# Performance work log

Hardware: AMD Instinct MI355X
Metric: run time of the kernel (lower is better)

Reference implementation:

```python
import jax, jax.numpy as jnp
import numpy as np

B, D, H, C = 8192, 384, 256, 6
K_MIN, K_MAX = 4, 16
LN_EPS = 1e-5


def setup_inputs() -> dict:
    key = jax.random.key(0)
    ks = jax.random.split(key, 6)
    s = lambda k, shape: (jax.random.normal(k, shape, jnp.float32) * 0.05)
    return {
        "x": jax.random.normal(ks[0], (B, D), jnp.float32),
        "W_proj": s(ks[1], (D, H)), "b_proj": jnp.zeros((H,), jnp.float32),
        "W_tau": s(ks[2], (D, 1)), "b_tau": jnp.zeros((1,), jnp.float32),
        "W_res": s(ks[3], (H, H)), "b_res": jnp.zeros((H,), jnp.float32),
        "ln_g": jnp.ones((H,), jnp.float32), "ln_b": jnp.zeros((H,), jnp.float32),
        "W_fc": s(ks[4], (H, C)), "b_fc": jnp.zeros((C,), jnp.float32),
    }


def reference(x, W_proj, b_proj, W_tau, b_tau, W_res, b_res, ln_g, ln_b, W_fc, b_fc):
    # adaptive k per sample (torch path casts to int -> non-differentiable)
    tau = jax.nn.sigmoid(x @ W_tau + b_tau)[:, 0]                      # [B]
    k = jax.lax.stop_gradient(
        jnp.clip(jnp.round(K_MAX - (K_MAX - K_MIN) * tau), 1, K_MAX)
    ).astype(jnp.int32)                                                # [B]

    # pairwise squared distances (same nearest-neighbor ordering as cdist)
    sq = jnp.sum(x * x, axis=-1)                                       # [B]
    d2 = sq[:, None] + sq[None, :] - 2.0 * (x @ x.T)                   # [B,B]
    _, idx = jax.lax.top_k(-jax.lax.stop_gradient(d2), K_MAX)          # [B,K_MAX] nearest (incl. self)

    h = jax.nn.relu(x @ W_proj + b_proj)                               # [B,H]

    # ragged top-k mean via fixed K_MAX gather + position mask
    gathered = h[idx]                                                  # [B,K_MAX,H]
    mask = (jnp.arange(K_MAX)[None, :] < k[:, None]).astype(h.dtype)   # [B,K_MAX]
    agg = jnp.einsum('bkh,bk->bh', gathered, mask) / k[:, None].astype(h.dtype)

    r = jax.nn.relu(agg @ W_res + b_res)                               # [B,H]
    z = h + r
    mu = jnp.mean(z, axis=-1, keepdims=True)
    var = jnp.var(z, axis=-1, keepdims=True)
    zn = (z - mu) / jnp.sqrt(var + LN_EPS)
    return (zn * ln_g + ln_b) @ W_fc + b_fc                            # [B,C]
```

## Files before the change

kernel.cpp:

```cpp
#include <hip/hip_runtime.h>
#include <hip/hip_fp16.h>
#include <math.h>

#define NROWS 8192
#define DDIM 384
#define HDIM 256
#define CDIM 6
#define LN_EPS 1e-5f
#define DSTR 138

typedef short bf16x8 __attribute__((ext_vector_type(8)));
typedef float f32x4 __attribute__((ext_vector_type(4)));
typedef unsigned short u16x8 __attribute__((ext_vector_type(8)));
typedef unsigned short u16x4 __attribute__((ext_vector_type(4)));
typedef unsigned short u16x2 __attribute__((ext_vector_type(2)));

__device__ __forceinline__ bool dj_better(float d1, int j1, float d2, int j2) {
    return (d1 < d2) || (d1 == d2 && j1 < j2);
}

__device__ __forceinline__ unsigned int umin_(unsigned int a, unsigned int b) { return a < b ? a : b; }
__device__ __forceinline__ unsigned int umax_(unsigned int a, unsigned int b) { return a > b ? a : b; }

__device__ __forceinline__ unsigned short map16f(float v) {
    union { _Float16 f; unsigned short u; } c;
    c.f = (_Float16)v;
    unsigned short b = c.u;
    return (unsigned short)(b ^ (unsigned short)((((short)b) >> 15) | 0x8000));
}

__device__ __forceinline__ float unmap16(unsigned int m16b) {
    unsigned short fb = (m16b & 0x8000u) ? (unsigned short)(m16b ^ 0x8000u)
                                         : (unsigned short)(~m16b);
    union { unsigned short u; _Float16 f; } cv; cv.u = fb;
    return (float)cv.f;
}

__device__ __forceinline__ unsigned short rne_bf16(float v) {
    unsigned int u = __float_as_uint(v);
    u += 0x7fffu + ((u >> 16) & 1u);
    return (unsigned short)(u >> 16);
}

__device__ __forceinline__ void ins8(
    unsigned int& s0, unsigned int& s1, unsigned int& s2, unsigned int& s3,
    unsigned int& s4, unsigned int& s5, unsigned int& s6, unsigned int& s7,
    unsigned int& m, unsigned int key)
{
    if (key < m) {
        s0 = (s0 == m) ? key : s0;
        s1 = (s1 == m) ? key : s1;
        s2 = (s2 == m) ? key : s2;
        s3 = (s3 == m) ? key : s3;
        s4 = (s4 == m) ? key : s4;
        s5 = (s5 == m) ? key : s5;
        s6 = (s6 == m) ? key : s6;
        s7 = (s7 == m) ? key : s7;
        m = umax_(umax_(umax_(s0, s1), umax_(s2, s3)),
                  umax_(umax_(s4, s5), umax_(s6, s7)));
    }
}

__device__ __forceinline__ unsigned int max8_(
    unsigned int s0, unsigned int s1, unsigned int s2, unsigned int s3,
    unsigned int s4, unsigned int s5, unsigned int s6, unsigned int s7)
{
    return umax_(umax_(umax_(s0, s1), umax_(s2, s3)),
                 umax_(umax_(s4, s5), umax_(s6, s7)));
}

__global__ void __launch_bounds__(256) prep_kernel(
    const float* __restrict__ x, const float* __restrict__ W_tau,
    const float* __restrict__ b_tau, unsigned short* __restrict__ xb,
    float* __restrict__ sq, int* __restrict__ kk,
    const float* __restrict__ Wp, unsigned short* __restrict__ wpT,
    const float* __restrict__ Wr, unsigned short* __restrict__ wrT)
{
    int tid = threadIdx.x;
    if (blockIdx.x < NROWS / 4) {
        int wave = tid >> 6, lane = tid & 63;
        int row = blockIdx.x * 4 + wave;
        const float* xr = x + (size_t)row * DDIM;
        unsigned short* xbr = xb + (size_t)row * DDIM;
        float s = 0.f, tp = 0.f;
        #pragma unroll
        for (int q = 0; q < 6; ++q) {
            float v = xr[lane + 64 * q];
            xbr[lane + 64 * q] = rne_bf16(v);
            s = fmaf(v, v, s);
            tp = fmaf(v, W_tau[lane + 64 * q], tp);
        }
        #pragma unroll
        for (int off = 32; off > 0; off >>= 1) {
            s += __shfl_xor(s, off);
            tp += __shfl_xor(tp, off);
        }
        if (lane == 0) {
            sq[row] = s;
            float u = tp + b_tau[0];
            float tau = 1.f / (1.f + expf(-u));
            float kf = rintf(16.f - 12.f * tau);
            int k = (int)kf;
            k = min(16, max(1, k));
            kk[row] = k;
        }
    } else {
        int i = (blockIdx.x - NROWS / 4) * 256 + tid;
        if (i < DDIM * HDIM) {
            int k = i / HDIM, n = i % HDIM;
            wpT[(size_t)n * DDIM + k] = rne_bf16(Wp[i]);
        } else {
            int j = i - DDIM * HDIM;
            if (j < HDIM * HDIM) {
                int k = j / HDIM, n = j % HDIM;
                wrT[(size_t)n * HDIM + k] = rne_bf16(Wr[j]);
            }
        }
    }
}

__global__ void __launch_bounds__(256) mfma_gemm_bias_relu_kernel(
    const unsigned short* __restrict__ A, const unsigned short* __restrict__ WT,
    const float* __restrict__ bias, float* __restrict__ out,
    unsigned short* __restrict__ hb, int K)
{
    __shared__ unsigned short Abuf[128 * 32];
    __shared__ unsigned short Bbuf[128 * 32];

    const int tid = threadIdx.x;
    const int wave = tid >> 6;
    const int rowbase = blockIdx.x * 128;
    const int nbase = blockIdx.y * 128;
    const int lane = tid & 63;
    const int wr = (wave >> 1) * 64;
    const int wc = (wave & 1) * 64;
    const int m16 = lane & 15;
    const int kq = lane >> 4;

    const int er0 = tid >> 2;
    const int er1 = 64 + (tid >> 2);
    const int eko = tid & 3;

    f32x4 acc[4][4];
    #pragma unroll
    for (int a = 0; a < 4; ++a)
        #pragma unroll
        for (int b = 0; b < 4; ++b)
            acc[a][b] = (f32x4){0.f, 0.f, 0.f, 0.f};

    for (int kb = 0; kb < K / 32; ++kb) {
        const int k0 = kb * 32;
        __syncthreads();
        __builtin_amdgcn_global_load_lds(
            (const __attribute__((address_space(1))) void*)(A + (size_t)(rowbase + er0) * K + k0 + eko * 8),
            (__attribute__((address_space(3))) void*)((char*)Abuf + (wave * 64) * 16), 16, 0, 0);
        __builtin_amdgcn_global_load_lds(
            (const __attribute__((address_space(1))) void*)(A + (size_t)(rowbase + er1) * K + k0 + eko * 8),
            (__attribute__((address_space(3))) void*)((char*)Abuf + (256 + wave * 64) * 16), 16, 0, 0);
        __builtin_amdgcn_global_load_lds(
            (const __attribute__((address_space(1))) void*)(WT + (size_t)(nbase + er0) * K + k0 + eko * 8),
            (__attribute__((address_space(3))) void*)((char*)Bbuf + (wave * 64) * 16), 16, 0, 0);
        __builtin_amdgcn_global_load_lds(
            (const __attribute__((address_space(1))) void*)(WT + (size_t)(nbase + er1) * K + k0 + eko * 8),
            (__attribute__((address_space(3))) void*)((char*)Bbuf + (256 + wave * 64) * 16), 16, 0, 0);
        __syncthreads();

        bf16x8 af[4], bfr[4];
        #pragma unroll
        for (int s = 0; s < 4; ++s) {
            af[s]  = *(const bf16x8*)&Abuf[(wr + s * 16 + m16) * 32 + kq * 8];
            bfr[s] = *(const bf16x8*)&Bbuf[(wc + s * 16 + m16) * 32 + kq * 8];
        }
        #pragma unroll
        for (int si = 0; si < 4; ++si)
            #pragma unroll
            for (int sj = 0; sj < 4; ++sj)
                acc[si][sj] = __builtin_amdgcn_mfma_f32_16x16x32_bf16(
                    af[si], bfr[sj], acc[si][sj], 0, 0, 0);
    }

    #pragma unroll
    for (int sj = 0; sj < 4; ++sj) {
        int c = nbase + wc + sj * 16 + m16;
        float bc = bias[c];
        #pragma unroll
        for (int si = 0; si < 4; ++si) {
            int r = rowbase + wr + si * 16 + kq * 4;
            #pragma unroll
            for (int v = 0; v < 4; ++v) {
                float val = fmaxf(acc[si][sj][v] + bc, 0.f);
                out[(size_t)(r + v) * HDIM + c] = val;
                if (hb) hb[(size_t)(r + v) * HDIM + c] = rne_bf16(val);
            }
        }
    }
}

__global__ void __launch_bounds__(256) dist_topk_kernel(
    const unsigned short* __restrict__ xb, const float* __restrict__ sq,
    unsigned int* __restrict__ keys)
{
    __shared__ unsigned short Abuf[128 * 32];
    __shared__ unsigned short Bbuf[128 * 32];
    __shared__ __align__(16) unsigned short Dt[128 * DSTR];

    int t = blockIdx.x;
    int bi = (int)((sqrtf(8.f * (float)t + 1.f) - 1.f) * 0.5f);
    while ((bi + 1) * (bi + 2) / 2 <= t) ++bi;
    while (bi * (bi + 1) / 2 > t) --bi;
    int bj = t - bi * (bi + 1) / 2;

    const int tid = threadIdx.x;
    const int wave = tid >> 6;
    const int lane = tid & 63;
    const int rowbase = bi * 128;
    const int colbase = bj * 128;
    const int wr = (wave >> 1) * 64;
    const int wc = (wave & 1) * 64;
    const int m16 = lane & 15;
    const int kq = lane >> 4;

    const int er0 = tid >> 2;
    const int er1 = 64 + (tid >> 2);
    const int eko = tid & 3;

    f32x4 acc[4][4];
    #pragma unroll
    for (int a = 0; a < 4; ++a)
        #pragma unroll
        for (int b = 0; b < 4; ++b)
            acc[a][b] = (f32x4){0.f, 0.f, 0.f, 0.f};

    for (int kb = 0; kb < DDIM / 32; ++kb) {
        const int k0 = kb * 32;
        __syncthreads();
        __builtin_amdgcn_global_load_lds(
            (const __attribute__((address_space(1))) void*)(xb + (size_t)(rowbase + er0) * DDIM + k0 + eko * 8),
            (__attribute__((address_space(3))) void*)((char*)Abuf + (wave * 64) * 16), 16, 0, 0);
        __builtin_amdgcn_global_load_lds(
            (const __attribute__((address_space(1))) void*)(xb + (size_t)(rowbase + er1) * DDIM + k0 + eko * 8),
            (__attribute__((address_space(3))) void*)((char*)Abuf + (256 + wave * 64) * 16), 16, 0, 0);
        __builtin_amdgcn_global_load_lds(
            (const __attribute__((address_space(1))) void*)(xb + (size_t)(colbase + er0) * DDIM + k0 + eko * 8),
            (__attribute__((address_space(3))) void*)((char*)Bbuf + (wave * 64) * 16), 16, 0, 0);
        __builtin_amdgcn_global_load_lds(
            (const __attribute__((address_space(1))) void*)(xb + (size_t)(colbase + er1) * DDIM + k0 + eko * 8),
            (__attribute__((address_space(3))) void*)((char*)Bbuf + (256 + wave * 64) * 16), 16, 0, 0);
        __syncthreads();

        bf16x8 af[4], bfr[4];
        #pragma unroll
        for (int s = 0; s < 4; ++s) {
            af[s]  = *(const bf16x8*)&Abuf[(wr + s * 16 + m16) * 32 + kq * 8];
            bfr[s] = *(const bf16x8*)&Bbuf[(wc + s * 16 + m16) * 32 + kq * 8];
        }
        #pragma unroll
        for (int si = 0; si < 4; ++si)
            #pragma unroll
            for (int sj = 0; sj < 4; ++sj)
                acc[si][sj] = __builtin_amdgcn_mfma_f32_16x16x32_bf16(
                    af[si], bfr[sj], acc[si][sj], 0, 0, 0);
    }

    const int sr = tid >> 1;
    const int seg = tid & 1;

    {
        float sqc[4];
        #pragma unroll
        for (int sj = 0; sj < 4; ++sj) sqc[sj] = sq[colbase + wc + sj * 16 + m16];
        #pragma unroll
        for (int si = 0; si < 4; ++si)
            #pragma unroll
            for (int sj = 0; sj < 4; ++sj) {
                int r = wr + si * 16 + kq * 4;
                int c = wc + sj * 16 + m16;
                #pragma unroll
                for (int v = 0; v < 4; ++v)
                    Dt[(r + v) * DSTR + c] = map16f(sqc[sj] - 2.0f * acc[si][sj][v]);
            }
        __syncthreads();

        const unsigned short* rowp = &Dt[sr * DSTR + seg * 64];
        const int cb0 = colbase + seg * 64;
        u16x8 c0 = *(const u16x8*)rowp;
        unsigned int s0 = ((unsigned int)c0[0] << 13) | (unsigned int)(cb0 + 0);
        unsigned int s1 = ((unsigned int)c0[1] << 13) | (unsigned int)(cb0 + 1);
        unsigned int s2 = ((unsigned int)c0[2] << 13) | (unsigned int)(cb0 + 2);
        unsigned int s3 = ((unsigned int)c0[3] << 13) | (unsigned int)(cb0 + 3);
        unsigned int s4 = ((unsigned int)c0[4] << 13) | (unsigned int)(cb0 + 4);
        unsigned int s5 = ((unsigned int)c0[5] << 13) | (unsigned int)(cb0 + 5);
        unsigned int s6 = ((unsigned int)c0[6] << 13) | (unsigned int)(cb0 + 6);
        unsigned int s7 = ((unsigned int)c0[7] << 13) | (unsigned int)(cb0 + 7);
        unsigned int m = max8_(s0, s1, s2, s3, s4, s5, s6, s7);
        #pragma unroll
        for (int i = 1; i < 8; ++i) {
            u16x8 ch = *(const u16x8*)(rowp + i * 8);
            u16x4 g4 = __builtin_elementwise_min(
                __builtin_shufflevector(ch, ch, 0, 1, 2, 3),
                __builtin_shufflevector(ch, ch, 4, 5, 6, 7));
            u16x2 g2 = __builtin_elementwise_min(
                __builtin_shufflevector(g4, g4, 0, 1),
                __builtin_shufflevector(g4, g4, 2, 3));
            unsigned int gmin = umin_((unsigned int)g2[0], (unsigned int)g2[1]);
            if ((gmin << 13) < m) {
                int cb = cb0 + i * 8;
                #pragma unroll
                for (int e = 0; e < 8; ++e)
                    ins8(s0, s1, s2, s3, s4, s5, s6, s7, m,
                         ((unsigned int)ch[e] << 13) | (unsigned int)(cb + e));
            }
        }
        size_t kb = (size_t)(rowbase + sr) * 1024 + (size_t)bj * 16 + seg * 8;
        uint4 o0; o0.x = s0; o0.y = s1; o0.z = s2; o0.w = s3;
        uint4 o1; o1.x = s4; o1.y = s5; o1.z = s6; o1.w = s7;
        *(uint4*)&keys[kb] = o0;
        *(uint4*)&keys[kb + 4] = o1;
    }

    if (bi != bj) {
        __syncthreads();
        #pragma unroll
        for (int si = 0; si < 4; ++si) {
            float4 sqr4 = *(const float4*)&sq[rowbase + wr + si * 16 + kq * 4];
            float srw[4] = {sqr4.x, sqr4.y, sqr4.z, sqr4.w};
            #pragma unroll
            for (int sj = 0; sj < 4; ++sj) {
                int r = wr + si * 16 + kq * 4;
                int c = wc + sj * 16 + m16;
                unsigned short h4[4];
                #pragma unroll
                for (int v = 0; v < 4; ++v)
                    h4[v] = map16f(srw[v] - 2.0f * acc[si][sj][v]);
                *(unsigned long long*)&Dt[c * DSTR + r] = *(unsigned long long*)h4;
            }
        }
        __syncthreads();

        const unsigned short* rowp = &Dt[sr * DSTR + seg * 64];
        const int cb0 = rowbase + seg * 64;
        u16x8 c0 = *(const u16x8*)rowp;
        unsigned int s0 = ((unsigned int)c0[0] << 13) | (unsigned int)(cb0 + 0);
        unsigned int s1 = ((unsigned int)c0[1] << 13) | (unsigned int)(cb0 + 1);
        unsigned int s2 = ((unsigned int)c0[2] << 13) | (unsigned int)(cb0 + 2);
        unsigned int s3 = ((unsigned int)c0[3] << 13) | (unsigned int)(cb0 + 3);
        unsigned int s4 = ((unsigned int)c0[4] << 13) | (unsigned int)(cb0 + 4);
        unsigned int s5 = ((unsigned int)c0[5] << 13) | (unsigned int)(cb0 + 5);
        unsigned int s6 = ((unsigned int)c0[6] << 13) | (unsigned int)(cb0 + 6);
        unsigned int s7 = ((unsigned int)c0[7] << 13) | (unsigned int)(cb0 + 7);
        unsigned int m = max8_(s0, s1, s2, s3, s4, s5, s6, s7);
        #pragma unroll
        for (int i = 1; i < 8; ++i) {
            u16x8 ch = *(const u16x8*)(rowp + i * 8);
            u16x4 g4 = __builtin_elementwise_min(
                __builtin_shufflevector(ch, ch, 0, 1, 2, 3),
                __builtin_shufflevector(ch, ch, 4, 5, 6, 7));
            u16x2 g2 = __builtin_elementwise_min(
                __builtin_shufflevector(g4, g4, 0, 1),
                __builtin_shufflevector(g4, g4, 2, 3));
            unsigned int gmin = umin_((unsigned int)g2[0], (unsigned int)g2[1]);
            if ((gmin << 13) < m) {
                int cb = cb0 + i * 8;
                #pragma unroll
                for (int e = 0; e < 8; ++e)
                    ins8(s0, s1, s2, s3, s4, s5, s6, s7, m,
                         ((unsigned int)ch[e] << 13) | (unsigned int)(cb + e));
            }
        }
        size_t kb = (size_t)(colbase + sr) * 1024 + (size_t)bi * 16 + seg * 8;
        uint4 o0; o0.x = s0; o0.y = s1; o0.z = s2; o0.w = s3;
        uint4 o1; o1.x = s4; o1.y = s5; o1.z = s6; o1.w = s7;
        *(uint4*)&keys[kb] = o0;
        *(uint4*)&keys[kb + 4] = o1;
    }
}

__global__ void __launch_bounds__(256) topk_rescore_agg_kernel(
    const unsigned int* __restrict__ keys, const float* __restrict__ x,
    const float* __restrict__ sq, const int* __restrict__ kk,
    const unsigned short* __restrict__ hb, unsigned short* __restrict__ aggb)
{
    const int w = threadIdx.x >> 6;
    const int row = blockIdx.x * 4 + w;
    const int lane = threadIdx.x & 63;
    __shared__ int sidx[4][16];

    const uint4* kp = (const uint4*)(keys + (size_t)row * 1024 + lane * 16);
    uint4 v0 = kp[0], v1 = kp[1];
    unsigned int s0 = v0.x, s1 = v0.y, s2 = v0.z, s3 = v0.w;
    unsigned int s4 = v1.x, s5 = v1.y, s6 = v1.z, s7 = v1.w;
    unsigned int m = max8_(s0, s1, s2, s3, s4, s5, s6, s7);
    #pragma unroll
    for (int q = 2; q < 4; ++q) {
        uint4 v = kp[q];
        unsigned int gmin = umin_(umin_(v.x, v.y), umin_(v.z, v.w));
        if (gmin < m) {
            ins8(s0, s1, s2, s3, s4, s5, s6, s7, m, v.x);
            ins8(s0, s1, s2, s3, s4, s5, s6, s7, m, v.y);
            ins8(s0, s1, s2, s3, s4, s5, s6, s7, m, v.z);
            ins8(s0, s1, s2, s3, s4, s5, s6, s7, m, v.w);
        }
    }
    unsigned int lmin = umin_(umin_(umin_(s0, s1), umin_(s2, s3)),
                              umin_(umin_(s4, s5), umin_(s6, s7)));
    unsigned int myout = 0;
    for (int t = 0; t < 32; ++t) {
        unsigned int wv = lmin;
        #pragma unroll
        for (int off = 32; off > 0; off >>= 1)
            wv = umin_(wv, (unsigned int)__shfl_xor((int)wv, off));
        if (lane == t) myout = wv;
        if (lmin == wv) {
            s0 = (s0 == wv) ? 0xFFFFFFFFu : s0;
            s1 = (s1 == wv) ? 0xFFFFFFFFu : s1;
            s2 = (s2 == wv) ? 0xFFFFFFFFu : s2;
            s3 = (s3 == wv) ? 0xFFFFFFFFu : s3;
            s4 = (s4 == wv) ? 0xFFFFFFFFu : s4;
            s5 = (s5 == wv) ? 0xFFFFFFFFu : s5;
            s6 = (s6 == wv) ? 0xFFFFFFFFu : s6;
            s7 = (s7 == wv) ? 0xFFFFFFFFu : s7;
            lmin = umin_(umin_(umin_(s0, s1), umin_(s2, s3)),
                         umin_(umin_(s4, s5), umin_(s6, s7)));
        }
    }
    int myj = (int)(myout & 8191u);
    float dscr = (lane < 32) ? unmap16(myout >> 13) : INFINITY;

    const float EPS2 = 2.5f;
    const int k = kk[row];
    float d_k   = __shfl(dscr, k);
    float d_km1 = __shfl(dscr, k - 1);
    bool cin = false, amb = false;
    if (lane < 32) {
        if (lane < k) { cin = (dscr + EPS2 <= d_k); amb = !cin; }
        else          { amb = (dscr < d_km1 + EPS2); }
    }
    unsigned long long cinmask = __ballot(cin);
    unsigned long long ambmask = __ballot(amb);
    int n_in = __popcll(cinmask);
    int msel = k - n_in;

    float d_ex = 0.f;
    if (msel > 0) {
        float xr[6];
        #pragma unroll
        for (int q = 0; q < 6; ++q) xr[q] = x[(size_t)row * DDIM + lane + 64 * q];
        float sqrow = sq[row];
        unsigned long long mm = ambmask;
        while (mm) {
            int c = (int)(__ffsll(mm) - 1);
            mm &= mm - 1;
            int j = __shfl(myj, c);
            const float* xc = x + (size_t)j * DDIM;
            float p = 0.f;
            #pragma unroll
            for (int q = 0; q < 6; ++q) p = fmaf(xr[q], xc[lane + 64 * q], p);
            #pragma unroll
            for (int off = 32; off > 0; off >>= 1) p += __shfl_xor(p, off);
            float d = sqrow + sq[j] - 2.f * p;
            if (lane == c) d_ex = d;
        }
        int selrank = 0;
        unsigned long long mm2 = ambmask;
        while (mm2) {
            int u = (int)(__ffsll(mm2) - 1);
            mm2 &= mm2 - 1;
            float du = __shfl(d_ex, u);
            int ju = __shfl(myj, u);
            if (u != lane && dj_better(du, ju, d_ex, myj)) ++selrank;
        }
        if (amb && selrank < msel)
            sidx[w][n_in + selrank] = myj;
    }
    if (cin) {
        int pos = __popcll(cinmask & ((1ull << lane) - 1ull));
        sidx[w][pos] = myj;
    }
    __syncthreads();

    float a0 = 0.f, a1 = 0.f, a2 = 0.f, a3 = 0.f;
    for (int t = 0; t < k; ++t) {
        uint2 v = *(const uint2*)(hb + (size_t)sidx[w][t] * HDIM + lane * 4);
        a0 += __uint_as_float(v.x << 16);
        a1 += __uint_as_float(v.x & 0xFFFF0000u);
        a2 += __uint_as_float(v.y << 16);
        a3 += __uint_as_float(v.y & 0xFFFF0000u);
    }
    float inv = 1.f / (float)k;
    unsigned int b0 = rne_bf16(a0 * inv);
    unsigned int b1 = rne_bf16(a1 * inv);
    unsigned int b2 = rne_bf16(a2 * inv);
    unsigned int b3 = rne_bf16(a3 * inv);
    uint2 o; o.x = b0 | (b1 << 16); o.y = b2 | (b3 << 16);
    *(uint2*)(aggb + (size_t)row * HDIM + lane * 4) = o;
}

__global__ void __launch_bounds__(256) ln_fc_kernel(
    const float* __restrict__ h, const float* __restrict__ r,
    const float* __restrict__ g, const float* __restrict__ bb,
    const float* __restrict__ W_fc, const float* __restrict__ b_fc,
    float* __restrict__ out)
{
    const int row = blockIdx.x * 4 + (threadIdx.x >> 6);
    const int lane = threadIdx.x & 63;
    const float* hp = h + (size_t)row * HDIM;
    const float* rp = r + (size_t)row * HDIM;

    float z[4];
    #pragma unroll
    for (int q = 0; q < 4; ++q)
        z[q] = hp[lane + 64 * q] + rp[lane + 64 * q];

    float s = z[0] + z[1] + z[2] + z[3];
    float s2 = z[0]*z[0] + z[1]*z[1] + z[2]*z[2] + z[3]*z[3];
    #pragma unroll
    for (int off = 32; off > 0; off >>= 1) {
        s += __shfl_xor(s, off);
        s2 += __shfl_xor(s2, off);
    }
    float mu = s / 256.f;
    float rstd = rsqrtf(s2 / 256.f - mu * mu + LN_EPS);

    float p[6] = {0.f, 0.f, 0.f, 0.f, 0.f, 0.f};
    #pragma unroll
    for (int q = 0; q < 4; ++q) {
        int i = lane + 64 * q;
        float val = (z[q] - mu) * rstd * g[i] + bb[i];
        #pragma unroll
        for (int c = 0; c < 6; ++c)
            p[c] = fmaf(val, W_fc[i * 6 + c], p[c]);
    }
    #pragma unroll
    for (int c = 0; c < 6; ++c)
        #pragma unroll
        for (int off = 32; off > 0; off >>= 1) p[c] += __shfl_xor(p[c], off);

    if (lane < 6) {
        float o = p[0];
        o = (lane == 1) ? p[1] : o;
        o = (lane == 2) ? p[2] : o;
        o = (lane == 3) ? p[3] : o;
        o = (lane == 4) ? p[4] : o;
        o = (lane == 5) ? p[5] : o;
        out[(size_t)row * CDIM + lane] = o + b_fc[lane];
    }
}

extern "C" void kernel_launch(void* const* d_in, const int* in_sizes, int n_in,
                              void* d_out, int out_size, void* d_ws, size_t ws_size,
                              hipStream_t stream) {
    const float* x      = (const float*)d_in[0];
    const float* W_proj = (const float*)d_in[1];
    const float* b_proj = (const float*)d_in[2];
    const float* W_tau  = (const float*)d_in[3];
    const float* b_tau  = (const float*)d_in[4];
    const float* W_res  = (const float*)d_in[5];
    const float* b_res  = (const float*)d_in[6];
    const float* ln_g   = (const float*)d_in[7];
    const float* ln_b   = (const float*)d_in[8];
    const float* W_fc   = (const float*)d_in[9];
    const float* b_fc   = (const float*)d_in[10];
    float* out = (float*)d_out;

    char* ws = (char*)d_ws;
    float* sq   = (float*)ws;                        ws += (size_t)NROWS * 4;
    int*   kk   = (int*)ws;                          ws += (size_t)NROWS * 4;
    float* h    = (float*)ws;                        ws += (size_t)NROWS * HDIM * 4;
    float* r    = (float*)ws;                        ws += (size_t)NROWS * HDIM * 4;
    unsigned short* xb   = (unsigned short*)ws;      ws += (size_t)NROWS * DDIM * 2;
    unsigned short* hbuf = (unsigned short*)ws;      ws += (size_t)NROWS * HDIM * 2;
    unsigned short* aggb = (unsigned short*)ws;      ws += (size_t)NROWS * HDIM * 2;
    unsigned short* wpT  = (unsigned short*)ws;      ws += (size_t)DDIM * HDIM * 2;
    unsigned short* wrT  = (unsigned short*)ws;      ws += (size_t)HDIM * HDIM * 2;
    ws = (char*)(((size_t)ws + 255) & ~(size_t)255);
    unsigned int* keys = (unsigned int*)ws;          ws += (size_t)NROWS * 1024 * 4;

    const int prepW = (DDIM * HDIM + HDIM * HDIM + 255) / 256;
    prep_kernel<<<NROWS / 4 + prepW, 256, 0, stream>>>(
        x, W_tau, b_tau, xb, sq, kk, W_proj, wpT, W_res, wrT);
    mfma_gemm_bias_relu_kernel<<<dim3(NROWS / 128, HDIM / 128), 256, 0, stream>>>(
        xb, wpT, b_proj, h, hbuf, DDIM);
    dist_topk_kernel<<<(NROWS/128) * (NROWS/128 + 1) / 2, 256, 0, stream>>>(xb, sq, keys);
    topk_rescore_agg_kernel<<<NROWS / 4, 256, 0, stream>>>(keys, x, sq, kk, hbuf, aggb);
    mfma_gemm_bias_relu_kernel<<<dim3(NROWS / 128, HDIM / 128), 256, 0, stream>>>(
        aggb, wrT, b_res, r, (unsigned short*)nullptr, HDIM);
    ln_fc_kernel<<<NROWS / 4, 256, 0, stream>>>(h, r, ln_g, ln_b, W_fc, b_fc, out);
}
```

Baseline: 230.5 us.

## Alias GEMM staging buffers with distance tile and use branchless sorted top-8 insertion

Aliases the A/B staging buffers onto the distance tile in shared memory, adding a barrier after the MMA loop so the reuse is safe. This shrinks per-block LDS footprint so more blocks can be resident. It also replaces the threshold-gated, divergent max-replace insertion with an initial sorting network followed by a branchless insertion into a sorted list for every candidate. That removes branch divergence but does more ALU work per element, since no chunk is skipped anymore.

```diff
diff --git a/kernel.cpp b/kernel.cpp
--- a/kernel.cpp
+++ b/kernel.cpp
@@ -69,6 +69,31 @@
                  umax_(umax_(s4, s5), umax_(s6, s7)));
 }
 
+__device__ __forceinline__ void sins8(
+    unsigned int& s0, unsigned int& s1, unsigned int& s2, unsigned int& s3,
+    unsigned int& s4, unsigned int& s5, unsigned int& s6, unsigned int& s7,
+    unsigned int key)
+{
+    unsigned int t = umin_(s0, key);
+    s0 = umax_(t, s1); t = umin_(t, s1);
+    s1 = umax_(t, s2); t = umin_(t, s2);
+    s2 = umax_(t, s3); t = umin_(t, s3);
+    s3 = umax_(t, s4); t = umin_(t, s4);
+    s4 = umax_(t, s5); t = umin_(t, s5);
+    s5 = umax_(t, s6); t = umin_(t, s6);
+    s6 = umax_(t, s7); s7 = umin_(t, s7);
+}
+
+#define CE_(a, b) { unsigned int hi_ = umax_(a, b), lo_ = umin_(a, b); a = hi_; b = lo_; }
+#define SORT8_DESC(s0, s1, s2, s3, s4, s5, s6, s7) \
+    CE_(s0, s1) CE_(s2, s3) CE_(s4, s5) CE_(s6, s7) \
+    CE_(s0, s2) CE_(s1, s3) CE_(s4, s6) CE_(s5, s7) \
+    CE_(s1, s2) CE_(s5, s6) CE_(s0, s4) CE_(s3, s7) \
+    CE_(s1, s5) CE_(s2, s6) \
+    CE_(s1, s4) CE_(s3, s6) \
+    CE_(s2, s4) CE_(s3, s5) \
+    CE_(s3, s4)
+
 __global__ void __launch_bounds__(256) prep_kernel(
     const float* __restrict__ x, const float* __restrict__ W_tau,
     const float* __restrict__ b_tau, unsigned short* __restrict__ xb,
@@ -200,9 +225,10 @@
     const unsigned short* __restrict__ xb, const float* __restrict__ sq,
     unsigned int* __restrict__ keys)
 {
-    __shared__ unsigned short Abuf[128 * 32];
-    __shared__ unsigned short Bbuf[128 * 32];
-    __shared__ __align__(16) unsigned short Dt[128 * DSTR];
+    __shared__ __align__(16) unsigned short SMEM[128 * DSTR];
+    unsigned short* Abuf = SMEM;
+    unsigned short* Bbuf = SMEM + 128 * 32;
+    unsigned short* Dt   = SMEM;
 
     int t = blockIdx.x;
     int bi = (int)((sqrtf(8.f * (float)t + 1.f) - 1.f) * 0.5f);
@@ -261,6 +287,7 @@
                 acc[si][sj] = __builtin_amdgcn_mfma_f32_16x16x32_bf16(
                     af[si], bfr[sj], acc[si][sj], 0, 0, 0);
     }
+    __syncthreads();
 
     const int sr = tid >> 1;
     const int seg = tid & 1;
@@ -292,24 +319,15 @@
         unsigned int s5 = ((unsigned int)c0[5] << 13) | (unsigned int)(cb0 + 5);
         unsigned int s6 = ((unsigned int)c0[6] << 13) | (unsigned int)(cb0 + 6);
         unsigned int s7 = ((unsigned int)c0[7] << 13) | (unsigned int)(cb0 + 7);
-        unsigned int m = max8_(s0, s1, s2, s3, s4, s5, s6, s7);
+        SORT8_DESC(s0, s1, s2, s3, s4, s5, s6, s7);
         #pragma unroll
         for (int i = 1; i < 8; ++i) {
             u16x8 ch = *(const u16x8*)(rowp + i * 8);
-            u16x4 g4 = __builtin_elementwise_min(
-                __builtin_shufflevector(ch, ch, 0, 1, 2, 3),
-                __builtin_shufflevector(ch, ch, 4, 5, 6, 7));
-            u16x2 g2 = __builtin_elementwise_min(
-                __builtin_shufflevector(g4, g4, 0, 1),
-                __builtin_shufflevector(g4, g4, 2, 3));
-            unsigned int gmin = umin_((unsigned int)g2[0], (unsigned int)g2[1]);
-            if ((gmin << 13) < m) {
-                int cb = cb0 + i * 8;
-                #pragma unroll
-                for (int e = 0; e < 8; ++e)
-                    ins8(s0, s1, s2, s3, s4, s5, s6, s7, m,
-                         ((unsigned int)ch[e] << 13) | (unsigned int)(cb + e));
-            }
+            int cb = cb0 + i * 8;
+            #pragma unroll
+            for (int e = 0; e < 8; ++e)
+                sins8(s0, s1, s2, s3, s4, s5, s6, s7,
+                      ((unsigned int)ch[e] << 13) | (unsigned int)(cb + e));
         }
         size_t kb = (size_t)(rowbase + sr) * 1024 + (size_t)bj * 16 + seg * 8;
         uint4 o0; o0.x = s0; o0.y = s1; o0.z = s2; o0.w = s3;
@@ -348,24 +366,15 @@
         unsigned int s5 = ((unsigned int)c0[5] << 13) | (unsigned int)(cb0 + 5);
         unsigned int s6 = ((unsigned int)c0[6] << 13) | (unsigned int)(cb0 + 6);
         unsigned int s7 = ((unsigned int)c0[7] << 13) | (unsigned int)(cb0 + 7);
-        unsigned int m = max8_(s0, s1, s2, s3, s4, s5, s6, s7);
+        SORT8_DESC(s0, s1, s2, s3, s4, s5, s6, s7);
         #pragma unroll
         for (int i = 1; i < 8; ++i) {
             u16x8 ch = *(const u16x8*)(rowp + i * 8);
-            u16x4 g4 = __builtin_elementwise_min(
-                __builtin_shufflevector(ch, ch, 0, 1, 2, 3),
-                __builtin_shufflevector(ch, ch, 4, 5, 6, 7));
-            u16x2 g2 = __builtin_elementwise_min(
-                __builtin_shufflevector(g4, g4, 0, 1),
-                __builtin_shufflevector(g4, g4, 2, 3));
-            unsigned int gmin = umin_((unsigned int)g2[0], (unsigned int)g2[1]);
-            if ((gmin << 13) < m) {
-                int cb = cb0 + i * 8;
-                #pragma unroll
-                for (int e = 0; e < 8; ++e)
-                    ins8(s0, s1, s2, s3, s4, s5, s6, s7, m,
-                         ((unsigned int)ch[e] << 13) | (unsigned int)(cb + e));
-            }
+            int cb = cb0 + i * 8;
+            #pragma unroll
+            for (int e = 0; e < 8; ++e)
+                sins8(s0, s1, s2, s3, s4, s5, s6, s7,
+                      ((unsigned int)ch[e] << 13) | (unsigned int)(cb + e));
         }
         size_t kb = (size_t)(colbase + sr) * 1024 + (size_t)bi * 16 + seg * 8;
         uint4 o0; o0.x = s0; o0.y = s1; o0.z = s2; o0.w = s3;
```

Result: no change. 229.3 us (-0.5%).
